# Kernel tuning notes

Measured on AMD Instinct MI355X. Metric: run time of the kernel, lower is better.

The kernel has to match this reference:

```python
import jax, jax.numpy as jnp
import numpy as np

B, C, H, W = 16, 1, 2048, 128
K8 = 8  # conv1/conv2 expand in_dim -> in_dim*8 channels


def setup_inputs() -> dict:
    key = jax.random.key(0)
    k = jax.random.split(key, 6)
    x = jax.random.normal(k[0], (B, C, H, W), dtype=jnp.float32)
    # 1x1 convs with in_channels=1 reduce to per-output-channel scale + bias
    w1 = jax.random.normal(k[1], (K8,), dtype=jnp.float32) * 0.5
    b1 = jax.random.normal(k[2], (K8,), dtype=jnp.float32) * 0.1
    w2 = jax.random.normal(k[3], (K8,), dtype=jnp.float32) * 0.5
    b2 = jax.random.normal(k[4], (K8,), dtype=jnp.float32) * 0.1
    gamma = jax.random.normal(k[5], (1,), dtype=jnp.float32) * 0.1
    return {"x": x, "w1": w1, "b1": b1, "w2": w2, "b2": b2, "gamma": gamma}


def reference(x, w1, b1, w2, b2, gamma):
    # x: (B,1,H,W)
    # conv1 / conv2: 1x1 conv, 1 -> 8 channels == scale+bias broadcast
    p1 = x * w1[None, :, None, None] + b1[None, :, None, None]  # (B,8,H,W)
    p2 = x * w2[None, :, None, None] + b2[None, :, None, None]  # (B,8,H,W)
    # proj_query: permute(0,2,1,3).reshape(B,H,8W)
    q = p1.transpose(0, 2, 1, 3).reshape(B, H, K8 * W)
    # proj_key: permute(0,1,3,2).reshape(B,8W,H)
    k_ = p2.transpose(0, 1, 3, 2).reshape(B, K8 * W, H)
    energy = jnp.einsum('bhd,bdg->bhg', q, k_)  # (B,H,H)
    mn = energy.min(axis=2, keepdims=True)
    mx = energy.max(axis=2, keepdims=True)
    energy = (energy - mn) / (mx - mn + 1e-8)
    attn = jax.nn.softmax(energy, axis=2)  # (B,H,H)
    # attention.reshape(B,1,H,H) @ x (B,1,H,W) -> (B,1,H,W)
    out = jnp.einsum('bhg,bgw->bhw', attn, x[:, 0])[:, None]
    return gamma * out + x
```

## Files before the change

### kernel.cpp

```cpp
#include <hip/hip_runtime.h>
#include <hip/hip_bf16.h>

#define B_ 16
#define H_ 2048
#define W_ 128

using f32x4  = __attribute__((ext_vector_type(4))) float;
using bf16x8 = __attribute__((ext_vector_type(8))) short;

#define GLOAD_LDS16(g, l) __builtin_amdgcn_global_load_lds( \
    (const __attribute__((address_space(1))) unsigned int*)(g), \
    (__attribute__((address_space(3))) unsigned int*)(l), 16, 0, 0)

__device__ inline short bf16bits(float f) {
    union { __hip_bfloat16 h; short s; } u;
    u.h = __float2bfloat16(f);
    return u.s;
}

__global__ __launch_bounds__(256) void prep(const float* __restrict__ x,
                                            const float* __restrict__ b1,
                                            const float* __restrict__ w2,
                                            short* __restrict__ Xbt,
                                            short* __restrict__ XTt,
                                            float* __restrict__ cs) {
    __shared__ short xs2[8192];
    int b  = blockIdx.x >> 5;
    int g0 = (blockIdx.x & 31) * 64;
    const float* xb = x + ((size_t)b * H_ + g0) * W_;
    short* outb = Xbt + (size_t)b * H_ * W_ + (size_t)g0 * W_;
    short* outt = XTt + (size_t)b * H_ * W_ + (size_t)g0 * W_;
    int t = threadIdx.x, seg = t & 15, row_l = t >> 4;
    float Cc = 0.f;
#pragma unroll
    for (int c = 0; c < 8; ++c) Cc += b1[c] * w2[c];

#pragma unroll
    for (int it = 0; it < 4; ++it) {
        int row = it * 16 + row_l;
        const float* src = xb + (size_t)row * W_ + seg * 8;
        float4 v0 = *reinterpret_cast<const float4*>(src);
        float4 v1 = *reinterpret_cast<const float4*>(src + 4);
        bf16x8 v;
        v[0] = bf16bits(v0.x); v[1] = bf16bits(v0.y);
        v[2] = bf16bits(v0.z); v[3] = bf16bits(v0.w);
        v[4] = bf16bits(v1.x); v[5] = bf16bits(v1.y);
        v[6] = bf16bits(v1.z); v[7] = bf16bits(v1.w);
        int chunk = (it * 4 + (seg >> 2)) * 64 + (seg & 3) * 16 + row_l;
        *reinterpret_cast<bf16x8*>(outb + (size_t)chunk * 8) = v;
        float s = v0.x + v0.y + v0.z + v0.w + v1.x + v1.y + v1.z + v1.w;
        s += __shfl_xor(s, 1); s += __shfl_xor(s, 2);
        s += __shfl_xor(s, 4); s += __shfl_xor(s, 8);
        if (seg == 0) cs[b * H_ + g0 + row] = Cc * s;
        int c8 = seg ^ ((row >> 3) & 3);
        *reinterpret_cast<bf16x8*>(&xs2[row * 128 + c8 * 8]) = v;
    }
    __syncthreads();
#pragma unroll
    for (int it2 = 0; it2 < 4; ++it2) {
        int c = it2 * 256 + t;
        int r = c & 15, qp = (c >> 4) & 3, nt2 = (c >> 6) & 7, kt = c >> 9;
        int w = nt2 * 16 + r, g = kt * 32 + qp * 8;
        int c8p = (w >> 3) ^ ((g >> 3) & 3);
        bf16x8 vv;
#pragma unroll
        for (int jj = 0; jj < 8; ++jj)
            vv[jj] = xs2[(g + jj) * 128 + c8p * 8 + (w & 7)];
        *reinterpret_cast<bf16x8*>(outt + (size_t)c * 8) = vv;
    }
}

__global__ __launch_bounds__(256, 2) void fused_attn(
    const float* __restrict__ x,
    const short* __restrict__ Xbt, const short* __restrict__ XTt,
    const float* __restrict__ cs,
    const float* __restrict__ w1, const float* __restrict__ w2,
    const float* __restrict__ gamma, float* __restrict__ out) {
    __shared__ __align__(16) char stgA[2][8192];
    __shared__ __align__(16) char stgV[2][8192];
    __shared__ __align__(16) char pb[2][4096];
    __shared__ float red_mn[2][2][2][16];
    __shared__ float red_mx[2][2][2][16];
    __shared__ float zred[2][2][2][16];

    float A = 0.f;
#pragma unroll
    for (int c = 0; c < 8; ++c) A += w1[c] * w2[c];

    int tid = threadIdx.x;
    int wv = tid >> 6, lane = tid & 63;
    int wh = wv >> 1, wg = wv & 1;
    int q = lane >> 4, r = lane & 15;

    int bid = blockIdx.x;
    int swz = (bid & 7) * 64 + (bid >> 3);
    int b = swz >> 5, hb = swz & 31;
    int h_base = hb * 64;

    const char* xbt = (const char*)(Xbt + (size_t)b * H_ * W_);
    const char* xtt = (const char*)(XTt + (size_t)b * H_ * W_);
    const float* csb = cs + b * H_;

    bf16x8 afr[2][4];
#pragma unroll
    for (int hf = 0; hf < 2; ++hf)
#pragma unroll
        for (int k = 0; k < 4; ++k)
            afr[hf][k] = *reinterpret_cast<const bf16x8*>(
                xbt + (((size_t)((h_base >> 4) + wh * 2 + hf) * 4 + k) * 64 + lane) * 16);

    float mnv[2] = {3.4e38f, 3.4e38f}, mxv[2] = {-3.4e38f, -3.4e38f};
    {
        const char* ga = xbt + wv * 2048 + lane * 16;
        char* la = stgA[0] + wv * 2048;
        GLOAD_LDS16(ga, la); GLOAD_LDS16(ga + 1024, la + 1024);
    }
    __syncthreads();
    float4 csv = *reinterpret_cast<const float4*>(csb + wg * 16 + q * 4);
    for (int t = 0; t < 64; ++t) {
        float4 csn = csv;
        if (t < 63) {
            const char* ga = xbt + (size_t)(t + 1) * 8192 + wv * 2048 + lane * 16;
            char* la = stgA[(t + 1) & 1] + wv * 2048;
            GLOAD_LDS16(ga, la); GLOAD_LDS16(ga + 1024, la + 1024);
            csn = *reinterpret_cast<const float4*>(csb + (t + 1) * 32 + wg * 16 + q * 4);
        }
        const char* sa = stgA[t & 1] + lane * 16;
        bf16x8 bfr[4];
#pragma unroll
        for (int k = 0; k < 4; ++k)
            bfr[k] = *reinterpret_cast<const bf16x8*>(sa + ((wg * 4 + k) * 64) * 16);
        f32x4 s0 = {0.f, 0.f, 0.f, 0.f}, s1 = {0.f, 0.f, 0.f, 0.f};
#pragma unroll
        for (int k = 0; k < 4; ++k) {
            s0 = __builtin_amdgcn_mfma_f32_16x16x32_bf16(bfr[k], afr[0][k], s0, 0, 0, 0);
            s1 = __builtin_amdgcn_mfma_f32_16x16x32_bf16(bfr[k], afr[1][k], s1, 0, 0, 0);
        }
#pragma unroll
        for (int reg = 0; reg < 4; ++reg) {
            float t0 = fmaf(A, s0[reg], csv[reg]);
            float t1 = fmaf(A, s1[reg], csv[reg]);
            mnv[0] = fminf(mnv[0], t0); mxv[0] = fmaxf(mxv[0], t0);
            mnv[1] = fminf(mnv[1], t1); mxv[1] = fmaxf(mxv[1], t1);
        }
        __syncthreads();
        csv = csn;
    }
#pragma unroll
    for (int hf = 0; hf < 2; ++hf) {
        mnv[hf] = fminf(mnv[hf], __shfl_xor(mnv[hf], 16));
        mnv[hf] = fminf(mnv[hf], __shfl_xor(mnv[hf], 32));
        mxv[hf] = fmaxf(mxv[hf], __shfl_xor(mxv[hf], 16));
        mxv[hf] = fmaxf(mxv[hf], __shfl_xor(mxv[hf], 32));
    }
    if (lane < 16) {
        red_mn[wh][0][wg][lane] = mnv[0]; red_mn[wh][1][wg][lane] = mnv[1];
        red_mx[wh][0][wg][lane] = mxv[0]; red_mx[wh][1][wg][lane] = mxv[1];
    }
    __syncthreads();
    const float LOG2E = 1.4426950408889634f;
    float c1[2], c0v[2], A1[2];
#pragma unroll
    for (int hf = 0; hf < 2; ++hf) {
        float mn = fminf(red_mn[wh][hf][0][r], red_mn[wh][hf][1][r]);
        float mx = fmaxf(red_mx[wh][hf][0][r], red_mx[wh][hf][1][r]);
        float inv = LOG2E / (mx - mn + 1e-8f);
        c1[hf] = inv; c0v[hf] = -mn * inv; A1[hf] = A * inv;
    }

    f32x4 o[2][4];
#pragma unroll
    for (int i = 0; i < 2; ++i)
#pragma unroll
        for (int j = 0; j < 4; ++j) o[i][j] = (f32x4){0.f, 0.f, 0.f, 0.f};
    float zacc[2] = {0.f, 0.f};
    {
        const char* ga = xbt + wv * 2048 + lane * 16;
        char* la = stgA[0] + wv * 2048;
        const char* gv = xtt + wv * 2048 + lane * 16;
        char* lv = stgV[0] + wv * 2048;
        GLOAD_LDS16(ga, la); GLOAD_LDS16(ga + 1024, la + 1024);
        GLOAD_LDS16(gv, lv); GLOAD_LDS16(gv + 1024, lv + 1024);
    }
    __syncthreads();
    csv = *reinterpret_cast<const float4*>(csb + wg * 16 + q * 4);
    for (int t = 0; t < 64; ++t) {
        float4 csn = csv;
        if (t < 63) {
            const char* ga = xbt + (size_t)(t + 1) * 8192 + wv * 2048 + lane * 16;
            char* la = stgA[(t + 1) & 1] + wv * 2048;
            const char* gv = xtt + (size_t)(t + 1) * 8192 + wv * 2048 + lane * 16;
            char* lv = stgV[(t + 1) & 1] + wv * 2048;
            GLOAD_LDS16(ga, la); GLOAD_LDS16(ga + 1024, la + 1024);
            GLOAD_LDS16(gv, lv); GLOAD_LDS16(gv + 1024, lv + 1024);
            csn = *reinterpret_cast<const float4*>(csb + (t + 1) * 32 + wg * 16 + q * 4);
        }
        const char* sa = stgA[t & 1] + lane * 16;
        bf16x8 bfr[4];
#pragma unroll
        for (int k = 0; k < 4; ++k)
            bfr[k] = *reinterpret_cast<const bf16x8*>(sa + ((wg * 4 + k) * 64) * 16);
        const char* sv = stgV[t & 1] + lane * 16;
        bf16x8 bt[4];
#pragma unroll
        for (int n = 0; n < 4; ++n)
            bt[n] = *reinterpret_cast<const bf16x8*>(sv + (((wg * 4 + n)) * 64) * 16);
        f32x4 s0 = {0.f, 0.f, 0.f, 0.f}, s1 = {0.f, 0.f, 0.f, 0.f};
#pragma unroll
        for (int k = 0; k < 4; ++k) {
            s0 = __builtin_amdgcn_mfma_f32_16x16x32_bf16(bfr[k], afr[0][k], s0, 0, 0, 0);
            s1 = __builtin_amdgcn_mfma_f32_16x16x32_bf16(bfr[k], afr[1][k], s1, 0, 0, 0);
        }
        char* pw = pb[t & 1];
#pragma unroll
        for (int hf = 0; hf < 2; ++hf) {
            f32x4 ss = hf ? s1 : s0;
            float e0 = exp2f(fmaf(ss[0], A1[hf], fmaf(csv[0], c1[hf], c0v[hf])));
            float e1 = exp2f(fmaf(ss[1], A1[hf], fmaf(csv[1], c1[hf], c0v[hf])));
            float e2 = exp2f(fmaf(ss[2], A1[hf], fmaf(csv[2], c1[hf], c0v[hf])));
            float e3 = exp2f(fmaf(ss[3], A1[hf], fmaf(csv[3], c1[hf], c0v[hf])));
            zacc[hf] += (e0 + e1) + (e2 + e3);
            unsigned d0 = (unsigned)(unsigned short)bf16bits(e0) |
                          ((unsigned)(unsigned short)bf16bits(e1) << 16);
            unsigned d1 = (unsigned)(unsigned short)bf16bits(e2) |
                          ((unsigned)(unsigned short)bf16bits(e3) << 16);
            uint2 dd; dd.x = d0; dd.y = d1;
            *reinterpret_cast<uint2*>(
                pw + (((wh * 2 + hf) * 64 + (wg * 2 + (q >> 1)) * 16 + r) * 16 + (q & 1) * 8)) = dd;
        }
        __syncthreads();
        bf16x8 pa0 = *reinterpret_cast<const bf16x8*>(pw + ((wh * 2 + 0) * 64 + lane) * 16);
        bf16x8 pa1 = *reinterpret_cast<const bf16x8*>(pw + ((wh * 2 + 1) * 64 + lane) * 16);
#pragma unroll
        for (int n = 0; n < 4; ++n) {
            o[0][n] = __builtin_amdgcn_mfma_f32_16x16x32_bf16(pa0, bt[n], o[0][n], 0, 0, 0);
            o[1][n] = __builtin_amdgcn_mfma_f32_16x16x32_bf16(pa1, bt[n], o[1][n], 0, 0, 0);
        }
        csv = csn;
    }

#pragma unroll
    for (int hf = 0; hf < 2; ++hf) {
        zacc[hf] += __shfl_xor(zacc[hf], 16);
        zacc[hf] += __shfl_xor(zacc[hf], 32);
    }
    if (lane < 16) {
        zred[wh][0][wg][lane] = zacc[0];
        zred[wh][1][wg][lane] = zacc[1];
    }
    __syncthreads();

    float g_ = gamma[0];
#pragma unroll
    for (int hf = 0; hf < 2; ++hf) {
#pragma unroll
        for (int reg = 0; reg < 4; ++reg) {
            int hq = q * 4 + reg;
            float z = zred[wh][hf][0][hq] + zred[wh][hf][1][hq];
            float sc = g_ / z;
            int h = h_base + wh * 32 + hf * 16 + hq;
#pragma unroll
            for (int n = 0; n < 4; ++n) {
                int w = wg * 64 + n * 16 + r;
                size_t idx = ((size_t)b * H_ + h) * W_ + w;
                out[idx] = fmaf(sc, o[hf][n][reg], x[idx]);
            }
        }
    }
}

extern "C" void kernel_launch(void* const* d_in, const int* in_sizes, int n_in,
                              void* d_out, int out_size, void* d_ws, size_t ws_size,
                              hipStream_t stream) {
    const float* x     = (const float*)d_in[0];
    const float* w1    = (const float*)d_in[1];
    const float* b1    = (const float*)d_in[2];
    const float* w2    = (const float*)d_in[3];
    const float* b2    = (const float*)d_in[4];
    const float* gamma = (const float*)d_in[5];
    float* out = (float*)d_out;
    (void)b2;

    char* ws = (char*)d_ws;
    const size_t XB_BYTES = (size_t)B_ * H_ * W_ * 2;
    short* Xbt = (short*)ws;
    short* XTt = (short*)(ws + XB_BYTES);
    float* cs  = (float*)(ws + 2 * XB_BYTES);

    prep<<<B_ * 32, 256, 0, stream>>>(x, b1, w2, Xbt, XTt, cs);
    fused_attn<<<B_ * H_ / 64, 256, 0, stream>>>(x, Xbt, XTt, cs, w1, w2, gamma, out);
}
```

Measured before the change: 178.6 us.

## Use 512-thread blocks with one 16-row tile per wave and manual pipelined barriers

Both kernels move from 256 to 512 threads per block. In fused_attn each wave now owns a single 16-row slice instead of two, so register pressure drops and occupancy can rise (launch bounds 512,4). The loop also replaces __syncthreads with explicit s_waitcnt and s_barrier calls, adds sched_barrier and s_setprio around the MFMA sections, and issues the next-tile prefetch unconditionally with wraparound. The prep transpose packs two columns per 32-bit LDS read. The cost is that each wave repeats the same B-fragment LDS loads for half as much math, which raises LDS traffic per FLOP, and the hand-tuned waitcnt counts must match the number of outstanding loads.

```diff
diff --git a/kernel.cpp b/kernel.cpp
--- a/kernel.cpp
+++ b/kernel.cpp
@@ -18,7 +18,7 @@
     return u.s;
 }
 
-__global__ __launch_bounds__(256) void prep(const float* __restrict__ x,
+__global__ __launch_bounds__(512) void prep(const float* __restrict__ x,
                                             const float* __restrict__ b1,
                                             const float* __restrict__ w2,
                                             short* __restrict__ Xbt,
@@ -30,14 +30,15 @@
     const float* xb = x + ((size_t)b * H_ + g0) * W_;
     short* outb = Xbt + (size_t)b * H_ * W_ + (size_t)g0 * W_;
     short* outt = XTt + (size_t)b * H_ * W_ + (size_t)g0 * W_;
-    int t = threadIdx.x, seg = t & 15, row_l = t >> 4;
+    int t = threadIdx.x;
     float Cc = 0.f;
 #pragma unroll
     for (int c = 0; c < 8; ++c) Cc += b1[c] * w2[c];
 
 #pragma unroll
-    for (int it = 0; it < 4; ++it) {
-        int row = it * 16 + row_l;
+    for (int half = 0; half < 2; ++half) {
+        int p = half * 512 + t;
+        int row = p >> 4, seg = p & 15;
         const float* src = xb + (size_t)row * W_ + seg * 8;
         float4 v0 = *reinterpret_cast<const float4*>(src);
         float4 v1 = *reinterpret_cast<const float4*>(src + 4);
@@ -46,9 +47,9 @@
         v[2] = bf16bits(v0.z); v[3] = bf16bits(v0.w);
         v[4] = bf16bits(v1.x); v[5] = bf16bits(v1.y);
         v[6] = bf16bits(v1.z); v[7] = bf16bits(v1.w);
-        int chunk = (it * 4 + (seg >> 2)) * 64 + (seg & 3) * 16 + row_l;
+        int chunk = ((row >> 4) * 4 + (seg >> 2)) * 64 + (seg & 3) * 16 + (row & 15);
         *reinterpret_cast<bf16x8*>(outb + (size_t)chunk * 8) = v;
-        float s = v0.x + v0.y + v0.z + v0.w + v1.x + v1.y + v1.z + v1.w;
+        float s = (v0.x + v0.y + v0.z + v0.w) + (v1.x + v1.y + v1.z + v1.w);
         s += __shfl_xor(s, 1); s += __shfl_xor(s, 2);
         s += __shfl_xor(s, 4); s += __shfl_xor(s, 8);
         if (seg == 0) cs[b * H_ + g0 + row] = Cc * s;
@@ -56,21 +57,25 @@
         *reinterpret_cast<bf16x8*>(&xs2[row * 128 + c8 * 8]) = v;
     }
     __syncthreads();
-#pragma unroll
-    for (int it2 = 0; it2 < 4; ++it2) {
-        int c = it2 * 256 + t;
-        int r = c & 15, qp = (c >> 4) & 3, nt2 = (c >> 6) & 7, kt = c >> 9;
-        int w = nt2 * 16 + r, g = kt * 32 + qp * 8;
-        int c8p = (w >> 3) ^ ((g >> 3) & 3);
-        bf16x8 vv;
-#pragma unroll
-        for (int jj = 0; jj < 8; ++jj)
-            vv[jj] = xs2[(g + jj) * 128 + c8p * 8 + (w & 7)];
-        *reinterpret_cast<bf16x8*>(outt + (size_t)c * 8) = vv;
-    }
-}
-
-__global__ __launch_bounds__(256, 2) void fused_attn(
+    {
+        int r2 = t & 7, qp = (t >> 3) & 3, nt2 = (t >> 5) & 7, kt = t >> 8;
+        int w0 = nt2 * 16 + r2 * 2;
+        int c8p = (w0 >> 3) ^ qp;
+        int gb = kt * 32 + qp * 8;
+        bf16x8 lo, hi;
+#pragma unroll
+        for (int jj = 0; jj < 8; ++jj) {
+            unsigned u = *reinterpret_cast<const unsigned*>(
+                &xs2[(gb + jj) * 128 + c8p * 8 + (w0 & 7)]);
+            lo[jj] = (short)(u & 0xffffu);
+            hi[jj] = (short)(u >> 16);
+        }
+        *reinterpret_cast<bf16x8*>(outt + (size_t)(t * 2) * 8) = lo;
+        *reinterpret_cast<bf16x8*>(outt + (size_t)(t * 2 + 1) * 8) = hi;
+    }
+}
+
+__global__ __launch_bounds__(512, 4) void fused_attn(
     const float* __restrict__ x,
     const short* __restrict__ Xbt, const short* __restrict__ XTt,
     const float* __restrict__ cs,
@@ -79,9 +84,9 @@
     __shared__ __align__(16) char stgA[2][8192];
     __shared__ __align__(16) char stgV[2][8192];
     __shared__ __align__(16) char pb[2][4096];
-    __shared__ float red_mn[2][2][2][16];
-    __shared__ float red_mx[2][2][2][16];
-    __shared__ float zred[2][2][2][16];
+    __shared__ float red_mn[4][2][16];
+    __shared__ float red_mx[4][2][16];
+    __shared__ float zred[4][2][16];
 
     float A = 0.f;
 #pragma unroll
@@ -101,170 +106,123 @@
     const char* xtt = (const char*)(XTt + (size_t)b * H_ * W_);
     const float* csb = cs + b * H_;
 
-    bf16x8 afr[2][4];
-#pragma unroll
-    for (int hf = 0; hf < 2; ++hf)
-#pragma unroll
-        for (int k = 0; k < 4; ++k)
-            afr[hf][k] = *reinterpret_cast<const bf16x8*>(
-                xbt + (((size_t)((h_base >> 4) + wh * 2 + hf) * 4 + k) * 64 + lane) * 16);
-
-    float mnv[2] = {3.4e38f, 3.4e38f}, mxv[2] = {-3.4e38f, -3.4e38f};
-    {
-        const char* ga = xbt + wv * 2048 + lane * 16;
-        char* la = stgA[0] + wv * 2048;
-        GLOAD_LDS16(ga, la); GLOAD_LDS16(ga + 1024, la + 1024);
-    }
-    __syncthreads();
+    bf16x8 afr[4];
+#pragma unroll
+    for (int k = 0; k < 4; ++k)
+        afr[k] = *reinterpret_cast<const bf16x8*>(
+            xbt + ((size_t)(((h_base >> 4) + wh) * 4 + k) * 64 + lane) * 16);
+
+    float mnv = 3.4e38f, mxv = -3.4e38f;
+    GLOAD_LDS16(xbt + wv * 1024 + lane * 16, stgA[0] + wv * 1024);
     float4 csv = *reinterpret_cast<const float4*>(csb + wg * 16 + q * 4);
     for (int t = 0; t < 64; ++t) {
-        float4 csn = csv;
-        if (t < 63) {
-            const char* ga = xbt + (size_t)(t + 1) * 8192 + wv * 2048 + lane * 16;
-            char* la = stgA[(t + 1) & 1] + wv * 2048;
-            GLOAD_LDS16(ga, la); GLOAD_LDS16(ga + 1024, la + 1024);
-            csn = *reinterpret_cast<const float4*>(csb + (t + 1) * 32 + wg * 16 + q * 4);
-        }
-        const char* sa = stgA[t & 1] + lane * 16;
-        bf16x8 bfr[4];
-#pragma unroll
-        for (int k = 0; k < 4; ++k)
-            bfr[k] = *reinterpret_cast<const bf16x8*>(sa + ((wg * 4 + k) * 64) * 16);
-        f32x4 s0 = {0.f, 0.f, 0.f, 0.f}, s1 = {0.f, 0.f, 0.f, 0.f};
+        int tn = (t + 1) & 63;
+        float4 csn = *reinterpret_cast<const float4*>(csb + tn * 32 + wg * 16 + q * 4);
+        GLOAD_LDS16(xbt + (size_t)tn * 8192 + wv * 1024 + lane * 16,
+                    stgA[tn & 1] + wv * 1024);
+        asm volatile("s_waitcnt vmcnt(2)" ::: "memory");
+        __builtin_amdgcn_s_barrier();
+        __builtin_amdgcn_sched_barrier(0);
+        const char* sa = stgA[t & 1];
+        f32x4 s = {0.f, 0.f, 0.f, 0.f};
+        __builtin_amdgcn_s_setprio(1);
 #pragma unroll
         for (int k = 0; k < 4; ++k) {
-            s0 = __builtin_amdgcn_mfma_f32_16x16x32_bf16(bfr[k], afr[0][k], s0, 0, 0, 0);
-            s1 = __builtin_amdgcn_mfma_f32_16x16x32_bf16(bfr[k], afr[1][k], s1, 0, 0, 0);
-        }
+            bf16x8 bfr = *reinterpret_cast<const bf16x8*>(sa + ((wg * 4 + k) * 64 + lane) * 16);
+            s = __builtin_amdgcn_mfma_f32_16x16x32_bf16(bfr, afr[k], s, 0, 0, 0);
+        }
+        __builtin_amdgcn_s_setprio(0);
 #pragma unroll
         for (int reg = 0; reg < 4; ++reg) {
-            float t0 = fmaf(A, s0[reg], csv[reg]);
-            float t1 = fmaf(A, s1[reg], csv[reg]);
-            mnv[0] = fminf(mnv[0], t0); mxv[0] = fmaxf(mxv[0], t0);
-            mnv[1] = fminf(mnv[1], t1); mxv[1] = fmaxf(mxv[1], t1);
-        }
-        __syncthreads();
+            float tv = fmaf(A, s[reg], csv[reg]);
+            mnv = fminf(mnv, tv); mxv = fmaxf(mxv, tv);
+        }
+        __builtin_amdgcn_s_barrier();
+        __builtin_amdgcn_sched_barrier(0);
         csv = csn;
     }
-#pragma unroll
-    for (int hf = 0; hf < 2; ++hf) {
-        mnv[hf] = fminf(mnv[hf], __shfl_xor(mnv[hf], 16));
-        mnv[hf] = fminf(mnv[hf], __shfl_xor(mnv[hf], 32));
-        mxv[hf] = fmaxf(mxv[hf], __shfl_xor(mxv[hf], 16));
-        mxv[hf] = fmaxf(mxv[hf], __shfl_xor(mxv[hf], 32));
-    }
-    if (lane < 16) {
-        red_mn[wh][0][wg][lane] = mnv[0]; red_mn[wh][1][wg][lane] = mnv[1];
-        red_mx[wh][0][wg][lane] = mxv[0]; red_mx[wh][1][wg][lane] = mxv[1];
-    }
+    mnv = fminf(mnv, __shfl_xor(mnv, 16)); mnv = fminf(mnv, __shfl_xor(mnv, 32));
+    mxv = fmaxf(mxv, __shfl_xor(mxv, 16)); mxv = fmaxf(mxv, __shfl_xor(mxv, 32));
+    if (lane < 16) { red_mn[wh][wg][lane] = mnv; red_mx[wh][wg][lane] = mxv; }
     __syncthreads();
     const float LOG2E = 1.4426950408889634f;
-    float c1[2], c0v[2], A1[2];
-#pragma unroll
-    for (int hf = 0; hf < 2; ++hf) {
-        float mn = fminf(red_mn[wh][hf][0][r], red_mn[wh][hf][1][r]);
-        float mx = fmaxf(red_mx[wh][hf][0][r], red_mx[wh][hf][1][r]);
-        float inv = LOG2E / (mx - mn + 1e-8f);
-        c1[hf] = inv; c0v[hf] = -mn * inv; A1[hf] = A * inv;
-    }
-
-    f32x4 o[2][4];
-#pragma unroll
-    for (int i = 0; i < 2; ++i)
-#pragma unroll
-        for (int j = 0; j < 4; ++j) o[i][j] = (f32x4){0.f, 0.f, 0.f, 0.f};
-    float zacc[2] = {0.f, 0.f};
-    {
-        const char* ga = xbt + wv * 2048 + lane * 16;
-        char* la = stgA[0] + wv * 2048;
-        const char* gv = xtt + wv * 2048 + lane * 16;
-        char* lv = stgV[0] + wv * 2048;
-        GLOAD_LDS16(ga, la); GLOAD_LDS16(ga + 1024, la + 1024);
-        GLOAD_LDS16(gv, lv); GLOAD_LDS16(gv + 1024, lv + 1024);
-    }
-    __syncthreads();
+    float mn = fminf(red_mn[wh][0][r], red_mn[wh][1][r]);
+    float mx = fmaxf(red_mx[wh][0][r], red_mx[wh][1][r]);
+    float inv = LOG2E / (mx - mn + 1e-8f);
+    float c1 = inv, c0v = -mn * inv, A1 = A * inv;
+
+    f32x4 o[4];
+#pragma unroll
+    for (int i = 0; i < 4; ++i) o[i] = (f32x4){0.f, 0.f, 0.f, 0.f};
+    float zacc = 0.f;
+    GLOAD_LDS16(xbt + wv * 1024 + lane * 16, stgA[0] + wv * 1024);
+    GLOAD_LDS16(xtt + wv * 1024 + lane * 16, stgV[0] + wv * 1024);
     csv = *reinterpret_cast<const float4*>(csb + wg * 16 + q * 4);
     for (int t = 0; t < 64; ++t) {
-        float4 csn = csv;
-        if (t < 63) {
-            const char* ga = xbt + (size_t)(t + 1) * 8192 + wv * 2048 + lane * 16;
-            char* la = stgA[(t + 1) & 1] + wv * 2048;
-            const char* gv = xtt + (size_t)(t + 1) * 8192 + wv * 2048 + lane * 16;
-            char* lv = stgV[(t + 1) & 1] + wv * 2048;
-            GLOAD_LDS16(ga, la); GLOAD_LDS16(ga + 1024, la + 1024);
-            GLOAD_LDS16(gv, lv); GLOAD_LDS16(gv + 1024, lv + 1024);
-            csn = *reinterpret_cast<const float4*>(csb + (t + 1) * 32 + wg * 16 + q * 4);
-        }
-        const char* sa = stgA[t & 1] + lane * 16;
-        bf16x8 bfr[4];
-#pragma unroll
-        for (int k = 0; k < 4; ++k)
-            bfr[k] = *reinterpret_cast<const bf16x8*>(sa + ((wg * 4 + k) * 64) * 16);
-        const char* sv = stgV[t & 1] + lane * 16;
+        int tn = (t + 1) & 63;
+        float4 csn = *reinterpret_cast<const float4*>(csb + tn * 32 + wg * 16 + q * 4);
+        GLOAD_LDS16(xbt + (size_t)tn * 8192 + wv * 1024 + lane * 16,
+                    stgA[tn & 1] + wv * 1024);
+        GLOAD_LDS16(xtt + (size_t)tn * 8192 + wv * 1024 + lane * 16,
+                    stgV[tn & 1] + wv * 1024);
+        asm volatile("s_waitcnt vmcnt(3)" ::: "memory");
+        __builtin_amdgcn_s_barrier();
+        __builtin_amdgcn_sched_barrier(0);
+        const char* sa = stgA[t & 1];
+        const char* sv = stgV[t & 1];
         bf16x8 bt[4];
 #pragma unroll
         for (int n = 0; n < 4; ++n)
-            bt[n] = *reinterpret_cast<const bf16x8*>(sv + (((wg * 4 + n)) * 64) * 16);
-        f32x4 s0 = {0.f, 0.f, 0.f, 0.f}, s1 = {0.f, 0.f, 0.f, 0.f};
+            bt[n] = *reinterpret_cast<const bf16x8*>(sv + ((wg * 4 + n) * 64 + lane) * 16);
+        f32x4 s = {0.f, 0.f, 0.f, 0.f};
+        __builtin_amdgcn_s_setprio(1);
 #pragma unroll
         for (int k = 0; k < 4; ++k) {
-            s0 = __builtin_amdgcn_mfma_f32_16x16x32_bf16(bfr[k], afr[0][k], s0, 0, 0, 0);
-            s1 = __builtin_amdgcn_mfma_f32_16x16x32_bf16(bfr[k], afr[1][k], s1, 0, 0, 0);
-        }
+            bf16x8 bfr = *reinterpret_cast<const bf16x8*>(sa + ((wg * 4 + k) * 64 + lane) * 16);
+            s = __builtin_amdgcn_mfma_f32_16x16x32_bf16(bfr, afr[k], s, 0, 0, 0);
+        }
+        __builtin_amdgcn_s_setprio(0);
+        float e0 = exp2f(fmaf(s[0], A1, fmaf(csv[0], c1, c0v)));
+        float e1 = exp2f(fmaf(s[1], A1, fmaf(csv[1], c1, c0v)));
+        float e2 = exp2f(fmaf(s[2], A1, fmaf(csv[2], c1, c0v)));
+        float e3 = exp2f(fmaf(s[3], A1, fmaf(csv[3], c1, c0v)));
+        zacc += (e0 + e1) + (e2 + e3);
+        unsigned d0 = (unsigned)(unsigned short)bf16bits(e0) |
+                      ((unsigned)(unsigned short)bf16bits(e1) << 16);
+        unsigned d1 = (unsigned)(unsigned short)bf16bits(e2) |
+                      ((unsigned)(unsigned short)bf16bits(e3) << 16);
+        uint2 dd; dd.x = d0; dd.y = d1;
         char* pw = pb[t & 1];
-#pragma unroll
-        for (int hf = 0; hf < 2; ++hf) {
-            f32x4 ss = hf ? s1 : s0;
-            float e0 = exp2f(fmaf(ss[0], A1[hf], fmaf(csv[0], c1[hf], c0v[hf])));
-            float e1 = exp2f(fmaf(ss[1], A1[hf], fmaf(csv[1], c1[hf], c0v[hf])));
-            float e2 = exp2f(fmaf(ss[2], A1[hf], fmaf(csv[2], c1[hf], c0v[hf])));
-            float e3 = exp2f(fmaf(ss[3], A1[hf], fmaf(csv[3], c1[hf], c0v[hf])));
-            zacc[hf] += (e0 + e1) + (e2 + e3);
-            unsigned d0 = (unsigned)(unsigned short)bf16bits(e0) |
-                          ((unsigned)(unsigned short)bf16bits(e1) << 16);
-            unsigned d1 = (unsigned)(unsigned short)bf16bits(e2) |
-                          ((unsigned)(unsigned short)bf16bits(e3) << 16);
-            uint2 dd; dd.x = d0; dd.y = d1;
-            *reinterpret_cast<uint2*>(
-                pw + (((wh * 2 + hf) * 64 + (wg * 2 + (q >> 1)) * 16 + r) * 16 + (q & 1) * 8)) = dd;
-        }
-        __syncthreads();
-        bf16x8 pa0 = *reinterpret_cast<const bf16x8*>(pw + ((wh * 2 + 0) * 64 + lane) * 16);
-        bf16x8 pa1 = *reinterpret_cast<const bf16x8*>(pw + ((wh * 2 + 1) * 64 + lane) * 16);
+        *reinterpret_cast<uint2*>(
+            pw + ((wh * 64 + (wg * 2 + (q >> 1)) * 16 + r) * 16 + (q & 1) * 8)) = dd;
+        asm volatile("s_waitcnt lgkmcnt(0)" ::: "memory");
+        __builtin_amdgcn_s_barrier();
+        __builtin_amdgcn_sched_barrier(0);
+        bf16x8 pa = *reinterpret_cast<const bf16x8*>(pw + (wh * 64 + lane) * 16);
+        __builtin_amdgcn_s_setprio(1);
+#pragma unroll
+        for (int n = 0; n < 4; ++n)
+            o[n] = __builtin_amdgcn_mfma_f32_16x16x32_bf16(pa, bt[n], o[n], 0, 0, 0);
+        __builtin_amdgcn_s_setprio(0);
+        csv = csn;
+    }
+
+    zacc += __shfl_xor(zacc, 16); zacc += __shfl_xor(zacc, 32);
+    if (lane < 16) zred[wh][wg][lane] = zacc;
+    __syncthreads();
+
+    float g_ = gamma[0];
+#pragma unroll
+    for (int reg = 0; reg < 4; ++reg) {
+        int hq = q * 4 + reg;
+        float z = zred[wh][0][hq] + zred[wh][1][hq];
+        float sc = g_ / z;
+        int h = h_base + wh * 16 + hq;
 #pragma unroll
         for (int n = 0; n < 4; ++n) {
-            o[0][n] = __builtin_amdgcn_mfma_f32_16x16x32_bf16(pa0, bt[n], o[0][n], 0, 0, 0);
-            o[1][n] = __builtin_amdgcn_mfma_f32_16x16x32_bf16(pa1, bt[n], o[1][n], 0, 0, 0);
-        }
-        csv = csn;
-    }
-
-#pragma unroll
-    for (int hf = 0; hf < 2; ++hf) {
-        zacc[hf] += __shfl_xor(zacc[hf], 16);
-        zacc[hf] += __shfl_xor(zacc[hf], 32);
-    }
-    if (lane < 16) {
-        zred[wh][0][wg][lane] = zacc[0];
-        zred[wh][1][wg][lane] = zacc[1];
-    }
-    __syncthreads();
-
-    float g_ = gamma[0];
-#pragma unroll
-    for (int hf = 0; hf < 2; ++hf) {
-#pragma unroll
-        for (int reg = 0; reg < 4; ++reg) {
-            int hq = q * 4 + reg;
-            float z = zred[wh][hf][0][hq] + zred[wh][hf][1][hq];
-            float sc = g_ / z;
-            int h = h_base + wh * 32 + hf * 16 + hq;
-#pragma unroll
-            for (int n = 0; n < 4; ++n) {
-                int w = wg * 64 + n * 16 + r;
-                size_t idx = ((size_t)b * H_ + h) * W_ + w;
-                out[idx] = fmaf(sc, o[hf][n][reg], x[idx]);
-            }
+            int w = wg * 64 + n * 16 + r;
+            size_t idx = ((size_t)b * H_ + h) * W_ + w;
+            out[idx] = fmaf(sc, o[n][reg], x[idx]);
         }
     }
 }
@@ -287,6 +245,6 @@
     short* XTt = (short*)(ws + XB_BYTES);
     float* cs  = (float*)(ws + 2 * XB_BYTES);
 
-    prep<<<B_ * 32, 256, 0, stream>>>(x, b1, w2, Xbt, XTt, cs);
-    fused_attn<<<B_ * H_ / 64, 256, 0, stream>>>(x, Xbt, XTt, cs, w1, w2, gamma, out);
-}
+    prep<<<B_ * 32, 512, 0, stream>>>(x, b1, w2, Xbt, XTt, cs);
+    fused_attn<<<B_ * H_ / 64, 512, 0, stream>>>(x, Xbt, XTt, cs, w1, w2, gamma, out);
+}
```

Result: faster. 163.9 us (-8.2%).
